# Optimization experiments

Measured on AMD Instinct MI355X. Metric: run time of the kernel, lower is better.

The kernel has to match this reference:

```python
import jax, jax.numpy as jnp
import numpy as np

N = 100_000      # nodes
E = 1_600_000    # edges (avg degree 16)
D_IN = 128
D_OUT = 128
K = 64           # low-rank attention rank


def setup_inputs() -> dict:
    key = jax.random.key(0)
    ks = jax.random.split(key, 6)
    s = lambda d: 1.0 / np.sqrt(d)
    return {
        "x": jax.random.normal(ks[0], (N, D_IN), dtype=jnp.float32),
        "edge_index": jax.random.randint(ks[1], (2, E), 0, N, dtype=jnp.int32),
        "W_gcn": jax.random.normal(ks[2], (D_IN, D_OUT), dtype=jnp.float32) * s(D_IN),
        "b_gcn": jnp.zeros((D_OUT,), jnp.float32),
        "W_att": jax.random.normal(ks[3], (D_IN, 4 * K), dtype=jnp.float32) * s(D_IN),
        "b_att": jnp.zeros((4 * K,), jnp.float32),
        "W_red": jax.random.normal(ks[4], (D_OUT + 2 * K, D_OUT), dtype=jnp.float32) * s(D_OUT + 2 * K),
        "b_red": jnp.zeros((D_OUT,), jnp.float32),
    }


def _forward(x, W_gcn, b_gcn, W_att, b_att, W_red, b_red, edge_index):
    n = x.shape[0]
    # --- GCN conv (symmetric normalization, self-loops), dropout = identity (eval) ---
    loop = jnp.arange(n, dtype=edge_index.dtype)
    src = jnp.concatenate([edge_index[0], loop])
    dst = jnp.concatenate([edge_index[1], loop])
    deg = jax.ops.segment_sum(jnp.ones_like(dst, dtype=x.dtype), dst, num_segments=n)
    dinv = jax.lax.rsqrt(deg)                      # deg >= 1 due to self-loops
    norm = dinv[src] * dinv[dst]                   # [E+n]
    h = x @ W_gcn                                  # [n, D_OUT]
    agg = jax.ops.segment_sum(h[src] * norm[:, None], dst, num_segments=n) + b_gcn
    x_local = jax.nn.relu(agg)

    # --- Low-rank global attention (LRGA) ---
    t = jax.nn.relu(x @ W_att + b_att)             # [n, 4K]
    U, V, Z, T = jnp.split(t, 4, axis=1)           # each [n, K]
    # joint_normalize2: scalar 1/mean(U @ (V^T @ 1_n))
    D = 1.0 / jnp.mean(U @ (V.T @ jnp.ones((n, 1), x.dtype)))
    res = (U @ (V.T @ Z)) * D                      # [n, K]
    x_global = jnp.concatenate([res, T], axis=1)   # [n, 2K]

    # --- fuse + dim reduce ---
    return jnp.concatenate([x_local, x_global], axis=1) @ W_red + b_red


def reference(x, edge_index, W_gcn, b_gcn, W_att, b_att, W_red, b_red):
    return _forward(x, W_gcn, b_gcn, W_att, b_att, W_red, b_red, edge_index)
```

## Files before the change

### kernel.cpp

```cpp
#include <hip/hip_runtime.h>

#define DIN   128
#define DOUT  128
#define KR    64
#define TCOLS 256
#define WCOLS 384
#define P_RED 1024
#define PSTR  4224
#define STCAP 6144

typedef unsigned short ushort_t;
typedef __attribute__((ext_vector_type(8))) short bf16x8;
typedef __attribute__((ext_vector_type(4))) float f32x4;

__device__ __forceinline__ float bf2f(unsigned short u) {
  return __uint_as_float(((unsigned int)u) << 16);
}
__device__ __forceinline__ unsigned short f2bf(float f) {
  unsigned int b = __float_as_uint(f);
  b = b + 0x7FFFu + ((b >> 16) & 1u);
  return (unsigned short)(b >> 16);
}

__global__ __launch_bounds__(256) void k_init(int* __restrict__ degc, float* __restrict__ VtZ,
                                              float* __restrict__ colsum, int* __restrict__ bcur,
                                              int* __restrict__ ocnt, int N) {
  int i = blockIdx.x * 256 + threadIdx.x;
  if (i < N) degc[i] = 1;
  if (i < 4096) VtZ[i] = 0.f;
  if (i < 128) colsum[i] = 0.f;
  if (i < 128) bcur[i] = 0;
  if (i == 0) ocnt[0] = 0;
}

__global__ __launch_bounds__(256) void k_split(const float* __restrict__ x,
                                               ushort_t* __restrict__ xhF, ushort_t* __restrict__ xloF,
                                               int N, int total_slots) {
  int gid = blockIdx.x * 256 + threadIdx.x;
  int stride = gridDim.x * 256;
  for (; gid < total_slots; gid += stride) {
    int f = gid >> 6, l = gid & 63;
    int r16 = f >> 2, s = f & 3;
    int row = r16 * 16 + (l & 15);
    int k = s * 32 + ((l >> 4) << 3);
    ushort4 h0, h1, l0, l1;
    if (row < N) {
      float4 a = *(const float4*)&x[(size_t)row * DIN + k];
      float4 b = *(const float4*)&x[(size_t)row * DIN + k + 4];
      h0.x = f2bf(a.x); h0.y = f2bf(a.y); h0.z = f2bf(a.z); h0.w = f2bf(a.w);
      h1.x = f2bf(b.x); h1.y = f2bf(b.y); h1.z = f2bf(b.z); h1.w = f2bf(b.w);
      l0.x = f2bf(a.x - bf2f(h0.x)); l0.y = f2bf(a.y - bf2f(h0.y));
      l0.z = f2bf(a.z - bf2f(h0.z)); l0.w = f2bf(a.w - bf2f(h0.w));
      l1.x = f2bf(b.x - bf2f(h1.x)); l1.y = f2bf(b.y - bf2f(h1.y));
      l1.z = f2bf(b.z - bf2f(h1.z)); l1.w = f2bf(b.w - bf2f(h1.w));
    } else {
      h0 = make_ushort4(0, 0, 0, 0); h1 = h0; l0 = h0; l1 = h0;
    }
    ((ushort4*)xhF)[gid * 2] = h0;
    ((ushort4*)xhF)[gid * 2 + 1] = h1;
    ((ushort4*)xloF)[gid * 2] = l0;
    ((ushort4*)xloF)[gid * 2 + 1] = l1;
  }
}

__global__ __launch_bounds__(256) void k_wprep(const float* __restrict__ Wg, const float* __restrict__ Wa,
                                               ushort_t* __restrict__ whF, ushort_t* __restrict__ wlF) {
  int g = blockIdx.x * 256 + threadIdx.x;
  int f = g >> 6, l = g & 63;
  int c16 = f >> 2, s = f & 3;
  int col = c16 * 16 + (l & 15);
  int k = s * 32 + ((l >> 4) << 3);
#pragma unroll
  for (int j = 0; j < 8; ++j) {
    float v = (col < DOUT) ? Wg[(size_t)(k + j) * DOUT + col]
                           : Wa[(size_t)(k + j) * TCOLS + (col - DOUT)];
    ushort_t h = f2bf(v);
    whF[(size_t)g * 8 + j] = h;
    wlF[(size_t)g * 8 + j] = f2bf(v - bf2f(h));
  }
}

__global__ __launch_bounds__(256) void k_scan1(const int* __restrict__ degc, int* __restrict__ offs,
                                               int* __restrict__ bsums, int N) {
  __shared__ int s[256];
  int tid = threadIdx.x;
  int base = blockIdx.x * 1024 + tid * 4;
  int c[4], e[4];
#pragma unroll
  for (int q = 0; q < 4; ++q) c[q] = (base + q < N) ? (degc[base + q] - 1) : 0;
  e[0] = 0; e[1] = c[0]; e[2] = e[1] + c[1]; e[3] = e[2] + c[2];
  int tsum = e[3] + c[3];
  s[tid] = tsum; __syncthreads();
  for (int off = 1; off < 256; off <<= 1) {
    int v = (tid >= off) ? s[tid - off] : 0;
    __syncthreads();
    s[tid] += v;
    __syncthreads();
  }
  int tb = s[tid] - tsum;
#pragma unroll
  for (int q = 0; q < 4; ++q) if (base + q < N) offs[base + q] = tb + e[q];
  if (tid == 255) bsums[blockIdx.x] = s[255];
}

__global__ __launch_bounds__(128) void k_scan2(const int* __restrict__ bsums, int* __restrict__ boff,
                                               int* __restrict__ offs, int NBLK, int N) {
  __shared__ int s[128];
  int tid = threadIdx.x;
  int v = (tid < NBLK) ? bsums[tid] : 0;
  s[tid] = v; __syncthreads();
  for (int off = 1; off < 128; off <<= 1) {
    int u = (tid >= off) ? s[tid - off] : 0;
    __syncthreads();
    s[tid] += u;
    __syncthreads();
  }
  boff[tid] = s[tid] - v;
  if (tid == 127) offs[N] = s[127];
}

__global__ __launch_bounds__(256) void k_scan3(int* __restrict__ offs, const int* __restrict__ boff,
                                               const int* __restrict__ degc, float* __restrict__ dinv,
                                               int* __restrict__ cursor, int N) {
  int i = blockIdx.x * 256 + threadIdx.x;
  if (i < N) {
    offs[i] += boff[i >> 10];
    dinv[i] = rsqrtf((float)degc[i]);
    cursor[i] = 0;
  }
}

__global__ __launch_bounds__(256) void k_bin(const int* __restrict__ ei, int* __restrict__ bcur,
                                             int* __restrict__ degc,
                                             int2* __restrict__ buckets,
                                             int2* __restrict__ oflow, int* __restrict__ ocnt,
                                             int E, int B, int CAP) {
  __shared__ int hist[128], pref[128], place[128], gbase[128];
  __shared__ int2 st[4096];
  int tid = threadIdx.x;
  int e0 = blockIdx.x * 4096;
  int nE = min(4096, E - e0);
  if (nE <= 0) return;

  if (tid < 128) { hist[tid] = 0; place[tid] = 0; }
  __syncthreads();

  int src[16], dst[16];
#pragma unroll
  for (int q = 0; q < 16; ++q) {
    int idx = tid + q * 256;
    if (idx < nE) {
      src[q] = ei[e0 + idx];
      dst[q] = ei[E + e0 + idx];
      atomicAdd(&hist[dst[q] >> 10], 1);
      atomicAdd(&degc[dst[q]], 1);
    }
  }
  __syncthreads();

  if (tid < 128) pref[tid] = hist[tid];
  __syncthreads();
  for (int off = 1; off < 128; off <<= 1) {
    int v = (tid < 128 && tid >= off) ? pref[tid - off] : 0;
    __syncthreads();
    if (tid < 128) pref[tid] += v;
    __syncthreads();
  }
  if (tid < 128) pref[tid] -= hist[tid];
  if (tid < B && hist[tid] > 0) gbase[tid] = atomicAdd(&bcur[tid], hist[tid]);
  __syncthreads();

#pragma unroll
  for (int q = 0; q < 16; ++q) {
    int idx = tid + q * 256;
    if (idx < nE) {
      int b = dst[q] >> 10;
      int p = pref[b] + atomicAdd(&place[b], 1);
      st[p] = make_int2(src[q], dst[q]);
    }
  }
  __syncthreads();

  for (int i = tid; i < nE; i += 256) {
    int2 q = st[i];
    int b = q.y >> 10;
    int gp = gbase[b] + (i - pref[b]);
    if (gp < CAP) {
      buckets[(size_t)b * CAP + gp] = q;
    } else {
      int oi = atomicAdd(ocnt, 1);
      oflow[oi] = q;
    }
  }
}

__global__ __launch_bounds__(256) void k_scatter2(const int2* __restrict__ buckets,
                                                  const int* __restrict__ bcur,
                                                  const int* __restrict__ offs,
                                                  const float* __restrict__ dinv,
                                                  int* __restrict__ cursor,
                                                  int2* __restrict__ csr, int CAP, int N) {
  __shared__ int lcur[256];
  __shared__ int2 st[STCAP];
  int cb = blockIdx.x >> 2;
  int lo = cb * 1024 + (blockIdx.x & 3) * 256;
  if (lo >= N) return;
  int tid = threadIdx.x;
  int nnode = min(256, N - lo);
  int base = offs[lo];
  int nb = offs[lo + nnode] - base;
  if (tid < nnode) lcur[tid] = offs[lo + tid];
  __syncthreads();
  int avail = min(bcur[cb], CAP);
  const int2* sp = &buckets[(size_t)cb * CAP];
  bool staged = (nb <= STCAP);
  int quarter = lo >> 8;
  for (int i = tid; i < avail; i += 256) {
    int2 q = sp[i];
    if ((q.y >> 8) != quarter) continue;
    int p = atomicAdd(&lcur[q.y - lo], 1);
    int2 c;
    c.x = q.x;
    c.y = __float_as_int(dinv[q.x] * dinv[q.y]);
    if (staged) st[p - base] = c;
    else        csr[p] = c;
  }
  __syncthreads();
  if (staged) {
    for (int i = tid; i < nb; i += 256) csr[base + i] = st[i];
  }
  if (tid < nnode) cursor[lo + tid] = lcur[tid];
}

__global__ __launch_bounds__(256) void k_fixup(const int2* __restrict__ oflow, const int* __restrict__ ocnt,
                                               int* __restrict__ cursor, const float* __restrict__ dinv,
                                               int2* __restrict__ csr) {
  int n = ocnt[0];
  for (int i = blockIdx.x * 256 + threadIdx.x; i < n; i += gridDim.x * 256) {
    int2 q = oflow[i];
    int pos = atomicAdd(&cursor[q.y], 1);
    int2 c;
    c.x = q.x;
    c.y = __float_as_int(dinv[q.x] * dinv[q.y]);
    csr[pos] = c;
  }
}

#define LOADK(S, AH, AL, BH, BL)                                              \
  {                                                                           \
    _Pragma("unroll") for (int m_ = 0; m_ < 4; ++m_) {                        \
      size_t fo_ = (((size_t)(r16b + m_) * 4 + (S)) * 64 + lane) * 8;         \
      AH[m_] = *(const bf16x8*)&xhF[fo_];                                     \
      AL[m_] = *(const bf16x8*)&xloF[fo_];                                    \
    }                                                                         \
    _Pragma("unroll") for (int n_ = 0; n_ < 4; ++n_) {                        \
      size_t fo_ = (((size_t)(c16b + n_) * 4 + (S)) * 64 + lane) * 8;         \
      BH[n_] = *(const bf16x8*)&whF[fo_];                                     \
      BL[n_] = *(const bf16x8*)&wlF[fo_];                                     \
    }                                                                         \
  }

__global__ __launch_bounds__(256) void k_gemm1_mfma(const ushort_t* __restrict__ xhF,
                                                    const ushort_t* __restrict__ xloF,
                                                    const ushort_t* __restrict__ whF,
                                                    const ushort_t* __restrict__ wlF,
                                                    const float* __restrict__ ba,
                                                    ushort_t* __restrict__ hs, ushort_t* __restrict__ t,
                                                    int N, int ntiles) {
  int bid = blockIdx.x;
  int g = bid / 24;
  int rem = bid - g * 24;
  int colblk = rem >> 3;
  int ytile = g * 8 + (rem & 7);
  if (ytile >= ntiles) return;

  int tid = threadIdx.x;
  int lane = tid & 63;
  int wave = tid >> 6;
  int wr = wave >> 1, wc = wave & 1;
  int rowbase = ytile * 128 + wr * 64;
  int gcb = colblk * 128 + wc * 64;
  int r16b = ytile * 8 + wr * 4;
  int c16b = colblk * 8 + wc * 4;
  int lr = lane & 15;
  int rq = (lane >> 4) * 4;

  f32x4 acc[4][4] = {};
  bf16x8 ah[2][4], al[2][4], bh[2][4], bl[2][4];

  LOADK(0, ah[0], al[0], bh[0], bl[0]);
#pragma unroll
  for (int s = 0; s < 4; ++s) {
    int cur = s & 1, nxt = cur ^ 1;
    if (s < 3) LOADK(s + 1, ah[nxt], al[nxt], bh[nxt], bl[nxt]);
#pragma unroll
    for (int m = 0; m < 4; ++m)
#pragma unroll
      for (int n = 0; n < 4; ++n) {
        acc[m][n] = __builtin_amdgcn_mfma_f32_16x16x32_bf16(ah[cur][m], bl[cur][n], acc[m][n], 0, 0, 0);
        acc[m][n] = __builtin_amdgcn_mfma_f32_16x16x32_bf16(al[cur][m], bh[cur][n], acc[m][n], 0, 0, 0);
        acc[m][n] = __builtin_amdgcn_mfma_f32_16x16x32_bf16(ah[cur][m], bh[cur][n], acc[m][n], 0, 0, 0);
      }
  }

  if (colblk == 0) {
#pragma unroll
    for (int m = 0; m < 4; ++m)
#pragma unroll
      for (int i = 0; i < 4; ++i) {
        int row = rowbase + m * 16 + rq + i;
        if (row < N) {
#pragma unroll
          for (int n = 0; n < 4; ++n)
            hs[(size_t)row * DOUT + gcb + n * 16 + lr] = f2bf(acc[m][n][i]);
        }
      }
  } else {
    float bav[4];
#pragma unroll
    for (int n = 0; n < 4; ++n) bav[n] = ba[gcb - DOUT + n * 16 + lr];
#pragma unroll
    for (int m = 0; m < 4; ++m)
#pragma unroll
      for (int i = 0; i < 4; ++i) {
        int row = rowbase + m * 16 + rq + i;
        if (row < N) {
#pragma unroll
          for (int n = 0; n < 4; ++n)
            t[(size_t)row * TCOLS + gcb - DOUT + n * 16 + lr] =
                f2bf(fmaxf(acc[m][n][i] + bav[n], 0.f));
        }
      }
  }
}

__global__ __launch_bounds__(256) void k_red(const ushort_t* __restrict__ t, float* __restrict__ part,
                                             int N) {
  __shared__ ushort_t ts[32 * 200];
  __shared__ float csh[512];
  int tid = threadIdx.x;
  int lane = tid & 63;
  int w = tid >> 6;
  int lr = lane & 15;
  int lk = (lane >> 4) * 8;
  int vcol = 64 + w * 16 + lr;
  int col2 = lane * 2;

  f32x4 acc[4] = {};
  float cs0 = 0.f, cs1 = 0.f;
  int ntiles = (N + 31) >> 5;

  for (int tile = blockIdx.x; tile < ntiles; tile += gridDim.x) {
    int r0 = tile * 32;
    for (int i = tid; i < 768; i += 256) {
      int r = i / 24, c0 = (i % 24) * 8;
      int row = r0 + r;
      ushort4 v0, v1;
      if (row < N) {
        v0 = ((const ushort4*)&t[(size_t)row * TCOLS + c0])[0];
        v1 = ((const ushort4*)&t[(size_t)row * TCOLS + c0])[1];
      } else {
        v0 = make_ushort4(0, 0, 0, 0); v1 = v0;
      }
      *(ushort4*)&ts[r * 200 + c0] = v0;
      *(ushort4*)&ts[r * 200 + c0 + 4] = v1;
    }
    __syncthreads();
    bf16x8 a, b[4];
#pragma unroll
    for (int j = 0; j < 8; ++j)
      ((ushort_t*)&a)[j] = ts[(lk + j) * 200 + vcol];
#pragma unroll
    for (int n = 0; n < 4; ++n)
#pragma unroll
      for (int j = 0; j < 8; ++j)
        ((ushort_t*)&b[n])[j] = ts[(lk + j) * 200 + 128 + n * 16 + lr];
#pragma unroll
    for (int j = 0; j < 8; ++j) {
      ushort2 u = *(const ushort2*)&ts[(w * 8 + j) * 200 + col2];
      cs0 += bf2f(u.x); cs1 += bf2f(u.y);
    }
#pragma unroll
    for (int n = 0; n < 4; ++n)
      acc[n] = __builtin_amdgcn_mfma_f32_16x16x32_bf16(a, b[n], acc[n], 0, 0, 0);
    __syncthreads();
  }

  float* pb = &part[(size_t)blockIdx.x * PSTR];
  int rq = (lane >> 4) * 4;
#pragma unroll
  for (int n = 0; n < 4; ++n)
#pragma unroll
    for (int i = 0; i < 4; ++i)
      pb[(w * 16 + rq + i) * 64 + n * 16 + lr] = acc[n][i];

  csh[tid] = cs0;
  csh[256 + tid] = cs1;
  __syncthreads();
  if (w == 0) {
    float t0 = csh[lane] + csh[64 + lane] + csh[128 + lane] + csh[192 + lane];
    float t1 = csh[256 + lane] + csh[320 + lane] + csh[384 + lane] + csh[448 + lane];
    pb[4096 + col2] = t0;
    pb[4096 + col2 + 1] = t1;
  }
}

__global__ __launch_bounds__(256) void k_redsum(const float* __restrict__ part,
                                                float* __restrict__ VtZ, float* __restrict__ colsum) {
  __shared__ float s[256];
  int tid = threadIdx.x;
  int j = blockIdx.x * 64 + (tid & 63);
  int bc = tid >> 6;
  float a = 0.f;
#pragma unroll 4
  for (int b = bc; b < P_RED; b += 4) a += part[(size_t)b * PSTR + j];
  s[tid] = a;
  __syncthreads();
  if (bc == 0) {
    float v = s[tid] + s[tid + 64] + s[tid + 128] + s[tid + 192];
    if (j < 4096) VtZ[j] = v;
    else colsum[j - 4096] = v;
  }
}

__global__ __launch_bounds__(64) void k_d(const float* __restrict__ colsum, float* __restrict__ Dws, int N) {
  __shared__ float s[64];
  int k = threadIdx.x;
  s[k] = colsum[k] * colsum[64 + k];
  __syncthreads();
  for (int off = 32; off > 0; off >>= 1) {
    if (k < off) s[k] += s[k + off];
    __syncthreads();
  }
  if (k == 0) {
    float p = s[0];
    Dws[0] = (p != 0.f) ? ((float)N / p) : 0.f;
  }
}

__global__ __launch_bounds__(256) void k_prep(const float* __restrict__ VtZ,
                                              const float* __restrict__ Dws,
                                              const float* __restrict__ Wr,
                                              ushort_t* __restrict__ weffF) {
  int g = blockIdx.x * 256 + threadIdx.x;
  int f = g >> 6, l = g & 63;
  int c16 = f >> 3, s = f & 7;
  int c = c16 * 16 + (l & 15);
  int k0 = s * 32 + ((l >> 4) << 3);
  float Dv = Dws[0];
#pragma unroll
  for (int j = 0; j < 8; ++j) {
    int k = k0 + j;
    float v;
    if (k < 128 || k >= 192) {
      v = Wr[(size_t)k * DOUT + c];
    } else {
      int kk = k - 128;
      float acc = 0.f;
      for (int q = 0; q < 64; ++q)
        acc += VtZ[kk * 64 + q] * Wr[(size_t)(128 + q) * DOUT + c];
      v = acc * Dv;
    }
    weffF[(size_t)g * 8 + j] = f2bf(v);
  }
}

__global__ __launch_bounds__(256) void k_aggout(const ushort_t* __restrict__ hs,
                                                const int2* __restrict__ csr,
                                                const int* __restrict__ offs,
                                                const float* __restrict__ dinv,
                                                const float* __restrict__ bg,
                                                const ushort_t* __restrict__ t,
                                                const ushort_t* __restrict__ weffF,
                                                const float* __restrict__ br,
                                                float* __restrict__ out, int N) {
  __shared__ ushort_t ys[32 * 264];
  int tid = threadIdx.x;
  int lane = tid & 63;
  int w = tid >> 6;
  int lr = lane & 15;
  int lk = (lane >> 4) * 8;
  int rq = (lane >> 4) * 4;
  int r0 = blockIdx.x * 32;
  int c2 = 2 * lane;

  float bg0 = bg[c2], bg1 = bg[c2 + 1];
  for (int q = 0; q < 8; ++q) {
    int r = w * 8 + q;
    int node = r0 + r;
    ushort2 o = make_ushort2(0, 0);
    if (node < N) {
      float dn = dinv[node];
      ushort2 u = *(const ushort2*)&hs[(size_t)node * DOUT + c2];
      float a0 = dn * dn * bf2f(u.x);
      float a1 = dn * dn * bf2f(u.y);
      int e = offs[node], e1 = offs[node + 1];
      for (; e + 4 <= e1; e += 4) {
        int2 q0 = csr[e], q1 = csr[e + 1], q2 = csr[e + 2], q3 = csr[e + 3];
        ushort2 r0v = *(const ushort2*)&hs[(size_t)q0.x * DOUT + c2];
        ushort2 r1v = *(const ushort2*)&hs[(size_t)q1.x * DOUT + c2];
        ushort2 r2v = *(const ushort2*)&hs[(size_t)q2.x * DOUT + c2];
        ushort2 r3v = *(const ushort2*)&hs[(size_t)q3.x * DOUT + c2];
        float n0 = __int_as_float(q0.y), n1 = __int_as_float(q1.y);
        float n2 = __int_as_float(q2.y), n3 = __int_as_float(q3.y);
        a0 += n0 * bf2f(r0v.x) + n1 * bf2f(r1v.x) + n2 * bf2f(r2v.x) + n3 * bf2f(r3v.x);
        a1 += n0 * bf2f(r0v.y) + n1 * bf2f(r1v.y) + n2 * bf2f(r2v.y) + n3 * bf2f(r3v.y);
      }
      for (; e < e1; ++e) {
        int2 qe = csr[e];
        ushort2 rv = *(const ushort2*)&hs[(size_t)qe.x * DOUT + c2];
        float n0 = __int_as_float(qe.y);
        a0 += n0 * bf2f(rv.x);
        a1 += n0 * bf2f(rv.y);
      }
      o.x = f2bf(fmaxf(a0 + bg0, 0.f));
      o.y = f2bf(fmaxf(a1 + bg1, 0.f));
    }
    *(ushort2*)&ys[r * 264 + c2] = o;
  }

  for (int i = tid; i < 512; i += 256) {
    int r = i >> 4, c0 = 128 + (i & 15) * 8;
    int row = r0 + r;
    ushort4 v0, v1;
    if (row < N) {
      const ushort_t* src = (c0 < 192) ? &t[(size_t)row * TCOLS + (c0 - 128)]
                                       : &t[(size_t)row * TCOLS + c0];
      v0 = ((const ushort4*)src)[0];
      v1 = ((const ushort4*)src)[1];
    } else {
      v0 = make_ushort4(0, 0, 0, 0); v1 = v0;
    }
    *(ushort4*)&ys[r * 264 + c0] = v0;
    *(ushort4*)&ys[r * 264 + c0 + 4] = v1;
  }
  __syncthreads();

  f32x4 acc[2][2] = {};
#pragma unroll
  for (int s = 0; s < 8; ++s) {
    bf16x8 a[2], b[2];
#pragma unroll
    for (int m = 0; m < 2; ++m)
      a[m] = *(const bf16x8*)&ys[(m * 16 + lr) * 264 + s * 32 + lk];
#pragma unroll
    for (int n = 0; n < 2; ++n) {
      int f = (w * 2 + n) * 8 + s;
      b[n] = *(const bf16x8*)&weffF[((size_t)f * 64 + lane) * 8];
    }
#pragma unroll
    for (int m = 0; m < 2; ++m)
#pragma unroll
      for (int n = 0; n < 2; ++n)
        acc[m][n] = __builtin_amdgcn_mfma_f32_16x16x32_bf16(a[m], b[n], acc[m][n], 0, 0, 0);
  }

  float brv[2];
#pragma unroll
  for (int n = 0; n < 2; ++n) brv[n] = br[w * 32 + n * 16 + lr];
#pragma unroll
  for (int m = 0; m < 2; ++m)
#pragma unroll
    for (int i = 0; i < 4; ++i) {
      int row = r0 + m * 16 + rq + i;
      if (row < N) {
#pragma unroll
        for (int n = 0; n < 2; ++n)
          out[(size_t)row * DOUT + w * 32 + n * 16 + lr] = acc[m][n][i] + brv[n];
      }
    }
}

extern "C" void kernel_launch(void* const* d_in, const int* in_sizes, int n_in,
                              void* d_out, int out_size, void* d_ws, size_t ws_size,
                              hipStream_t stream) {
  const float* x  = (const float*)d_in[0];
  const int* ei   = (const int*)d_in[1];
  const float* Wg = (const float*)d_in[2];
  const float* bg = (const float*)d_in[3];
  const float* Wa = (const float*)d_in[4];
  const float* ba = (const float*)d_in[5];
  const float* Wr = (const float*)d_in[6];
  const float* br = (const float*)d_in[7];
  float* out = (float*)d_out;

  const int N = in_sizes[0] / DIN;
  const int E = in_sizes[1] / 2;

  const int NT128 = (N + 127) / 128;
  const int N16P = NT128 * 8;
  const int NFRAG_A = N16P * 4;
  const int B = (N + 1023) >> 10;
  const int CAP = ((E / (B > 0 ? B : 1)) * 3 / 2 + 255) & ~255;

  char* p = (char*)d_ws;
  auto alloc = [&](size_t bytes) {
    char* r = p;
    p += (bytes + 255) & ~(size_t)255;
    return r;
  };
  float* Dws    = (float*)alloc(256);
  float* colsum = (float*)alloc(128 * 4);
  float* VtZ    = (float*)alloc(4096 * 4);
  int*   bsums  = (int*)alloc(1024);
  int*   boff   = (int*)alloc(1024);
  int*   bcur   = (int*)alloc(1024);
  int*   ocnt   = (int*)alloc(256);
  ushort_t* weffF = (ushort_t*)alloc(128 * 256 * 2);
  ushort_t* whF = (ushort_t*)alloc((size_t)24 * 4 * 512 * 2);
  ushort_t* wlF = (ushort_t*)alloc((size_t)24 * 4 * 512 * 2);
  float* part   = (float*)alloc((size_t)P_RED * PSTR * 4);
  int*   degc   = (int*)alloc((size_t)N * 4);
  float* dinv   = (float*)alloc((size_t)N * 4);
  int*   offs   = (int*)alloc((size_t)(N + 1) * 4);
  int*   cursor = (int*)alloc((size_t)N * 4);
  int2*  csr    = (int2*)alloc((size_t)E * 8);
  int2*  buckets= (int2*)alloc((size_t)B * CAP * 8);
  int2*  oflow  = (int2*)alloc((size_t)E * 8);
  ushort_t* xhF = (ushort_t*)alloc((size_t)NFRAG_A * 512 * 2);
  ushort_t* xloF= (ushort_t*)alloc((size_t)NFRAG_A * 512 * 2);
  ushort_t* hs  = (ushort_t*)alloc((size_t)N * DOUT * 2);
  ushort_t* t   = (ushort_t*)alloc((size_t)N * TCOLS * 2);
  (void)ws_size; (void)n_in; (void)out_size;

  const int GN = (N + 255) / 256;
  const int NBLK = (N + 1023) / 1024;
  const int G1 = ((NT128 + 7) / 8) * 24;
  const int GBIN = (E + 4095) / 4096;
  const int NT32 = (N + 31) / 32;

  k_init<<<GN, 256, 0, stream>>>(degc, VtZ, colsum, bcur, ocnt, N);
  k_bin<<<GBIN, 256, 0, stream>>>(ei, bcur, degc, buckets, oflow, ocnt, E, B, CAP);
  k_split<<<2048, 256, 0, stream>>>(x, xhF, xloF, N, NFRAG_A * 64);
  k_wprep<<<24, 256, 0, stream>>>(Wg, Wa, whF, wlF);
  k_scan1<<<NBLK, 256, 0, stream>>>(degc, offs, bsums, N);
  k_scan2<<<1, 128, 0, stream>>>(bsums, boff, offs, NBLK, N);
  k_scan3<<<GN, 256, 0, stream>>>(offs, boff, degc, dinv, cursor, N);
  k_scatter2<<<B * 4, 256, 0, stream>>>(buckets, bcur, offs, dinv, cursor, csr, CAP, N);
  k_fixup<<<32, 256, 0, stream>>>(oflow, ocnt, cursor, dinv, csr);
  k_gemm1_mfma<<<G1, 256, 0, stream>>>(xhF, xloF, whF, wlF, ba, hs, t, N, NT128);
  k_red<<<P_RED, 256, 0, stream>>>(t, part, N);
  k_redsum<<<PSTR / 64, 256, 0, stream>>>(part, VtZ, colsum);
  k_d<<<1, 64, 0, stream>>>(colsum, Dws, N);
  k_prep<<<16, 256, 0, stream>>>(VtZ, Dws, Wr, weffF);
  k_aggout<<<NT32, 256, 0, stream>>>(hs, csr, offs, dinv, bg, t, weffF, br, out, N);
}
```

Baseline: 428.0 us.

## Fold overflow fixup into scatter, double-buffer k_red, fuse D into k_prep

Removes the separate overflow fixup kernel and the global cursor array: each scatter block now processes overflow edges belonging to its quarter using its shared-memory cursors. k_red gets double-buffered shared-memory staging so the next tile loads while the current one computes, and the partial-sum block count is halved. The scalar D computation is folded into k_prep (done redundantly per block), eliminating k_d. In k_aggout the t-column staging is moved ahead of the aggregation loop to overlap loads. Every scatter block now scans the whole overflow list, which could cost more if overflow is large.

```diff
diff --git a/kernel.cpp b/kernel.cpp
--- a/kernel.cpp
+++ b/kernel.cpp
@@ -5,7 +5,7 @@
 #define KR    64
 #define TCOLS 256
 #define WCOLS 384
-#define P_RED 1024
+#define P_RED 512
 #define PSTR  4224
 #define STCAP 6144
 
@@ -121,12 +121,11 @@
 
 __global__ __launch_bounds__(256) void k_scan3(int* __restrict__ offs, const int* __restrict__ boff,
                                                const int* __restrict__ degc, float* __restrict__ dinv,
-                                               int* __restrict__ cursor, int N) {
+                                               int N) {
   int i = blockIdx.x * 256 + threadIdx.x;
   if (i < N) {
     offs[i] += boff[i >> 10];
     dinv[i] = rsqrtf((float)degc[i]);
-    cursor[i] = 0;
   }
 }
 
@@ -198,7 +197,8 @@
                                                   const int* __restrict__ bcur,
                                                   const int* __restrict__ offs,
                                                   const float* __restrict__ dinv,
-                                                  int* __restrict__ cursor,
+                                                  const int2* __restrict__ oflow,
+                                                  const int* __restrict__ ocnt,
                                                   int2* __restrict__ csr, int CAP, int N) {
   __shared__ int lcur[256];
   __shared__ int2 st[STCAP];
@@ -229,20 +229,16 @@
   if (staged) {
     for (int i = tid; i < nb; i += 256) csr[base + i] = st[i];
   }
-  if (tid < nnode) cursor[lo + tid] = lcur[tid];
-}
-
-__global__ __launch_bounds__(256) void k_fixup(const int2* __restrict__ oflow, const int* __restrict__ ocnt,
-                                               int* __restrict__ cursor, const float* __restrict__ dinv,
-                                               int2* __restrict__ csr) {
+  __syncthreads();
   int n = ocnt[0];
-  for (int i = blockIdx.x * 256 + threadIdx.x; i < n; i += gridDim.x * 256) {
+  for (int i = tid; i < n; i += 256) {
     int2 q = oflow[i];
-    int pos = atomicAdd(&cursor[q.y], 1);
+    if ((q.y >> 8) != quarter) continue;
+    int p = atomicAdd(&lcur[q.y - lo], 1);
     int2 c;
     c.x = q.x;
     c.y = __float_as_int(dinv[q.x] * dinv[q.y]);
-    csr[pos] = c;
+    csr[p] = c;
   }
 }
 
@@ -334,9 +330,27 @@
   }
 }
 
+#define STAGE_RED(BUF, TILE)                                                     \
+  {                                                                              \
+    int r0_ = (TILE) * 32;                                                       \
+    for (int i_ = tid; i_ < 768; i_ += 256) {                                    \
+      int r_ = i_ / 24, c0_ = (i_ % 24) * 8;                                     \
+      int row_ = r0_ + r_;                                                       \
+      ushort4 v0_, v1_;                                                          \
+      if (row_ < N) {                                                            \
+        v0_ = ((const ushort4*)&t[(size_t)row_ * TCOLS + c0_])[0];               \
+        v1_ = ((const ushort4*)&t[(size_t)row_ * TCOLS + c0_])[1];               \
+      } else {                                                                   \
+        v0_ = make_ushort4(0, 0, 0, 0); v1_ = v0_;                               \
+      }                                                                          \
+      *(ushort4*)&ts[BUF][r_ * 200 + c0_] = v0_;                                 \
+      *(ushort4*)&ts[BUF][r_ * 200 + c0_ + 4] = v1_;                             \
+    }                                                                            \
+  }
+
 __global__ __launch_bounds__(256) void k_red(const ushort_t* __restrict__ t, float* __restrict__ part,
                                              int N) {
-  __shared__ ushort_t ts[32 * 200];
+  __shared__ ushort_t ts[2][32 * 200];
   __shared__ float csh[512];
   int tid = threadIdx.x;
   int lane = tid & 63;
@@ -349,41 +363,34 @@
   f32x4 acc[4] = {};
   float cs0 = 0.f, cs1 = 0.f;
   int ntiles = (N + 31) >> 5;
-
-  for (int tile = blockIdx.x; tile < ntiles; tile += gridDim.x) {
-    int r0 = tile * 32;
-    for (int i = tid; i < 768; i += 256) {
-      int r = i / 24, c0 = (i % 24) * 8;
-      int row = r0 + r;
-      ushort4 v0, v1;
-      if (row < N) {
-        v0 = ((const ushort4*)&t[(size_t)row * TCOLS + c0])[0];
-        v1 = ((const ushort4*)&t[(size_t)row * TCOLS + c0])[1];
-      } else {
-        v0 = make_ushort4(0, 0, 0, 0); v1 = v0;
-      }
-      *(ushort4*)&ts[r * 200 + c0] = v0;
-      *(ushort4*)&ts[r * 200 + c0 + 4] = v1;
-    }
-    __syncthreads();
+  int cur = 0;
+
+  int tile = blockIdx.x;
+  if (tile < ntiles) STAGE_RED(0, tile);
+  __syncthreads();
+  for (; tile < ntiles; tile += gridDim.x) {
+    int nxt = tile + gridDim.x;
+    if (nxt < ntiles) STAGE_RED(cur ^ 1, nxt);
+    const ushort_t* tb = ts[cur];
     bf16x8 a, b[4];
 #pragma unroll
     for (int j = 0; j < 8; ++j)
-      ((ushort_t*)&a)[j] = ts[(lk + j) * 200 + vcol];
+      ((ushort_t*)&a)[j] = tb[(lk + j) * 200 + vcol];
 #pragma unroll
     for (int n = 0; n < 4; ++n)
 #pragma unroll
       for (int j = 0; j < 8; ++j)
-        ((ushort_t*)&b[n])[j] = ts[(lk + j) * 200 + 128 + n * 16 + lr];
+        ((ushort_t*)&b[n])[j] = tb[(lk + j) * 200 + 128 + n * 16 + lr];
 #pragma unroll
     for (int j = 0; j < 8; ++j) {
-      ushort2 u = *(const ushort2*)&ts[(w * 8 + j) * 200 + col2];
+      ushort2 u = *(const ushort2*)&tb[(w * 8 + j) * 200 + col2];
       cs0 += bf2f(u.x); cs1 += bf2f(u.y);
     }
 #pragma unroll
     for (int n = 0; n < 4; ++n)
       acc[n] = __builtin_amdgcn_mfma_f32_16x16x32_bf16(a, b[n], acc[n], 0, 0, 0);
     __syncthreads();
+    cur ^= 1;
   }
 
   float* pb = &part[(size_t)blockIdx.x * PSTR];
@@ -423,31 +430,29 @@
   }
 }
 
-__global__ __launch_bounds__(64) void k_d(const float* __restrict__ colsum, float* __restrict__ Dws, int N) {
-  __shared__ float s[64];
-  int k = threadIdx.x;
-  s[k] = colsum[k] * colsum[64 + k];
-  __syncthreads();
-  for (int off = 32; off > 0; off >>= 1) {
-    if (k < off) s[k] += s[k + off];
-    __syncthreads();
-  }
-  if (k == 0) {
-    float p = s[0];
-    Dws[0] = (p != 0.f) ? ((float)N / p) : 0.f;
-  }
-}
-
 __global__ __launch_bounds__(256) void k_prep(const float* __restrict__ VtZ,
-                                              const float* __restrict__ Dws,
+                                              const float* __restrict__ colsum,
                                               const float* __restrict__ Wr,
-                                              ushort_t* __restrict__ weffF) {
-  int g = blockIdx.x * 256 + threadIdx.x;
+                                              ushort_t* __restrict__ weffF, int N) {
+  __shared__ float dsh[64];
+  __shared__ float Dsh;
+  int tid = threadIdx.x;
+  if (tid < 64) dsh[tid] = colsum[tid] * colsum[64 + tid];
+  __syncthreads();
+  if (tid == 0) {
+    float p = 0.f;
+#pragma unroll 8
+    for (int i = 0; i < 64; ++i) p += dsh[i];
+    Dsh = (p != 0.f) ? ((float)N / p) : 0.f;
+  }
+  __syncthreads();
+  float Dv = Dsh;
+
+  int g = blockIdx.x * 256 + tid;
   int f = g >> 6, l = g & 63;
   int c16 = f >> 3, s = f & 7;
   int c = c16 * 16 + (l & 15);
   int k0 = s * 32 + ((l >> 4) << 3);
-  float Dv = Dws[0];
 #pragma unroll
   for (int j = 0; j < 8; ++j) {
     int k = k0 + j;
@@ -483,6 +488,22 @@
   int rq = (lane >> 4) * 4;
   int r0 = blockIdx.x * 32;
   int c2 = 2 * lane;
+
+  for (int i = tid; i < 512; i += 256) {
+    int r = i >> 4, c0 = 128 + (i & 15) * 8;
+    int row = r0 + r;
+    ushort4 v0, v1;
+    if (row < N) {
+      const ushort_t* src = (c0 < 192) ? &t[(size_t)row * TCOLS + (c0 - 128)]
+                                       : &t[(size_t)row * TCOLS + c0];
+      v0 = ((const ushort4*)src)[0];
+      v1 = ((const ushort4*)src)[1];
+    } else {
+      v0 = make_ushort4(0, 0, 0, 0); v1 = v0;
+    }
+    *(ushort4*)&ys[r * 264 + c0] = v0;
+    *(ushort4*)&ys[r * 264 + c0 + 4] = v1;
+  }
 
   float bg0 = bg[c2], bg1 = bg[c2 + 1];
   for (int q = 0; q < 8; ++q) {
@@ -518,22 +539,6 @@
     }
     *(ushort2*)&ys[r * 264 + c2] = o;
   }
-
-  for (int i = tid; i < 512; i += 256) {
-    int r = i >> 4, c0 = 128 + (i & 15) * 8;
-    int row = r0 + r;
-    ushort4 v0, v1;
-    if (row < N) {
-      const ushort_t* src = (c0 < 192) ? &t[(size_t)row * TCOLS + (c0 - 128)]
-                                       : &t[(size_t)row * TCOLS + c0];
-      v0 = ((const ushort4*)src)[0];
-      v1 = ((const ushort4*)src)[1];
-    } else {
-      v0 = make_ushort4(0, 0, 0, 0); v1 = v0;
-    }
-    *(ushort4*)&ys[r * 264 + c0] = v0;
-    *(ushort4*)&ys[r * 264 + c0 + 4] = v1;
-  }
   __syncthreads();
 
   f32x4 acc[2][2] = {};
@@ -599,7 +604,6 @@
     p += (bytes + 255) & ~(size_t)255;
     return r;
   };
-  float* Dws    = (float*)alloc(256);
   float* colsum = (float*)alloc(128 * 4);
   float* VtZ    = (float*)alloc(4096 * 4);
   int*   bsums  = (int*)alloc(1024);
@@ -613,7 +617,6 @@
   int*   degc   = (int*)alloc((size_t)N * 4);
   float* dinv   = (float*)alloc((size_t)N * 4);
   int*   offs   = (int*)alloc((size_t)(N + 1) * 4);
-  int*   cursor = (int*)alloc((size_t)N * 4);
   int2*  csr    = (int2*)alloc((size_t)E * 8);
   int2*  buckets= (int2*)alloc((size_t)B * CAP * 8);
   int2*  oflow  = (int2*)alloc((size_t)E * 8);
@@ -635,13 +638,11 @@
   k_wprep<<<24, 256, 0, stream>>>(Wg, Wa, whF, wlF);
   k_scan1<<<NBLK, 256, 0, stream>>>(degc, offs, bsums, N);
   k_scan2<<<1, 128, 0, stream>>>(bsums, boff, offs, NBLK, N);
-  k_scan3<<<GN, 256, 0, stream>>>(offs, boff, degc, dinv, cursor, N);
-  k_scatter2<<<B * 4, 256, 0, stream>>>(buckets, bcur, offs, dinv, cursor, csr, CAP, N);
-  k_fixup<<<32, 256, 0, stream>>>(oflow, ocnt, cursor, dinv, csr);
+  k_scan3<<<GN, 256, 0, stream>>>(offs, boff, degc, dinv, N);
+  k_scatter2<<<B * 4, 256, 0, stream>>>(buckets, bcur, offs, dinv, oflow, ocnt, csr, CAP, N);
   k_gemm1_mfma<<<G1, 256, 0, stream>>>(xhF, xloF, whF, wlF, ba, hs, t, N, NT128);
   k_red<<<P_RED, 256, 0, stream>>>(t, part, N);
   k_redsum<<<PSTR / 64, 256, 0, stream>>>(part, VtZ, colsum);
-  k_d<<<1, 64, 0, stream>>>(colsum, Dws, N);
-  k_prep<<<16, 256, 0, stream>>>(VtZ, Dws, Wr, weffF);
+  k_prep<<<16, 256, 0, stream>>>(VtZ, colsum, Wr, weffF, N);
   k_aggout<<<NT32, 256, 0, stream>>>(hs, csr, offs, dinv, bg, t, weffF, br, out, N);
 }
```

New measurement: 418.7 us, median of 2. -2.2%, faster.
